# Kernel tuning notes

Measured on AMD Instinct MI355X. Metric: run time of the kernel, lower is better.

## Reference

```python
import jax, jax.numpy as jnp
import numpy as np

PSZ = 3      # patch_size
TOPK = 2     # topk candidates
EPS = 1e-12  # F.normalize eps


def extract_patches(x, psz, stride):
    """Torch unfold-style patch extraction: (B,C,H,W) -> (B, nH*nW, C, psz, psz)."""
    B, C, H, W = x.shape
    nH = (H - psz) // stride + 1
    nW = (W - psz) // stride + 1
    slices = []
    for di in range(psz):          # fixed 3x3 loop, not a data-dim loop
        for dj in range(psz):
            slices.append(x[:, :, di:di + (nH - 1) * stride + 1:stride,
                                  dj:dj + (nW - 1) * stride + 1:stride])
    p = jnp.stack(slices, axis=-1)                      # (B,C,nH,nW,psz*psz)
    p = p.reshape(B, C, nH, nW, psz, psz)
    p = p.transpose(0, 2, 3, 1, 4, 5).reshape(B, nH * nW, C, psz, psz)
    return p


def l2_normalize(x, axis):
    n = jnp.sqrt(jnp.sum(x * x, axis=axis, keepdims=True))
    return x / jnp.maximum(n, EPS)


def setup_inputs() -> dict:
    key = jax.random.key(0)
    k1, k2 = jax.random.split(key)
    pred_style = jax.random.normal(k1, (2, 128, 48, 48), dtype=jnp.float32)
    target_style = jax.random.normal(k2, (2 * TOPK, 128, 48, 48), dtype=jnp.float32)
    return {"pred_style": pred_style, "target_style": target_style}


def reference(pred_style, target_style):
    B = pred_style.shape[0]
    # raw patches (used for the final MSE / gather)
    tp = extract_patches(target_style, PSZ, 1)   # (B*TOPK, nT, C, 3, 3)
    pp = extract_patches(pred_style, PSZ, 1)     # (B, nQ, C, 3, 3)
    nT = tp.shape[1]

    # matching is done on channel-normalized features (F.normalize dim=1 / dim=2)
    p1n = extract_patches(l2_normalize(pred_style, axis=1), PSZ, 1)  # (B,nQ,C,3,3)
    tpn = l2_normalize(tp, axis=2).reshape(B, TOPK, nT, *tp.shape[2:])

    # cosine cross-correlation == conv with candidate patches as filters
    scores = jnp.einsum('bqcij,bkncij->bknq', p1n, tpn)  # (B,TOPK,nT,nQ)->(B,TOPK,nQ) reduce below

    sv = jnp.max(scores, axis=2)      # (B, TOPK, nQ) best value per candidate set
    si = jnp.argmax(scores, axis=2)   # (B, TOPK, nQ) best spatial idx per k
    k_idx = jnp.argmax(sv, axis=1)    # (B, nQ) best k per query position
    spatial = jnp.take_along_axis(si, k_idx[:, None, :], axis=1)[:, 0]  # (B, nQ)

    tpr = tp.reshape(B, TOPK, nT, *tp.shape[2:])
    bi = jnp.arange(B)[:, None]
    gathered = tpr[bi, k_idx, spatial]  # (B, nQ, C, 3, 3)

    return jnp.mean((pp - gathered) ** 2)
```

## Files before the change

kernel.cpp:

```cpp
#include <hip/hip_runtime.h>
#include <hip/hip_bf16.h>

typedef unsigned short u16;
typedef __attribute__((ext_vector_type(8))) short short8;
typedef __attribute__((ext_vector_type(4))) float f32x4;
typedef __attribute__((ext_vector_type(4))) unsigned int u32x4;

#define CC    128
#define WW    48
#define HW2   2304
#define NHW   46
#define NQ    2116
#define NPIX  2304
#define DSTRIDE ((size_t)NPIX * NPIX + 64)
#define BATCH 2

__device__ __forceinline__ u16 f2bf(float f) {
  union { float f; unsigned u; } x; x.f = f;
  unsigned r = (x.u + 0x7fffu + ((x.u >> 16) & 1u)) >> 16;
  return (u16)r;
}
__device__ __forceinline__ float b2f(u16 v) {
  union { unsigned u; float f; } x; x.u = ((unsigned)v) << 16;
  return x.f;
}

__global__ __launch_bounds__(256) void k_norm(const float* __restrict__ pred,
                                              const float* __restrict__ targ,
                                              u16* __restrict__ PnT, u16* __restrict__ TnT) {
  const int img = blockIdx.y;
  const int p0  = blockIdx.x * 64;
  const int tid = threadIdx.x;
  const float* src = img < 2 ? pred + (size_t)img * CC * HW2
                             : targ + (size_t)(img - 2) * CC * HW2;
  u16* out = img < 2 ? PnT + (size_t)img * NPIX * CC
                     : TnT + (size_t)(img - 2) * NPIX * CC;

  __shared__ float sT[64][129];
  __shared__ float sInv[64];

  #pragma unroll
  for (int it = 0; it < 32; ++it) {
    int idx = it * 256 + tid;
    int c = idx >> 6, p = idx & 63;
    sT[p][c] = src[(size_t)c * HW2 + p0 + p];
  }
  __syncthreads();
  if (tid < 64) {
    float s = 0.f;
    for (int c = 0; c < CC; ++c) { float v = sT[tid][c]; s += v * v; }
    sInv[tid] = 1.0f / fmaxf(sqrtf(s), 1e-12f);
  }
  __syncthreads();
  #pragma unroll
  for (int it = 0; it < 4; ++it) {
    int cid = it * 256 + tid;
    int p = cid >> 4, g = cid & 15;
    int r = p0 + p;
    int sc = (g & ~7) | ((g & 7) ^ (r & 7));
    float inv = sInv[p];
    unsigned pack[4];
    #pragma unroll
    for (int e = 0; e < 8; ++e) {
      float v = sT[p][sc * 8 + e] * inv;
      if ((e & 1) == 0) pack[e >> 1] = (unsigned)f2bf(v);
      else              pack[e >> 1] |= ((unsigned)f2bf(v)) << 16;
    }
    u32x4 o; o.x = pack[0]; o.y = pack[1]; o.z = pack[2]; o.w = pack[3];
    *reinterpret_cast<u32x4*>(out + (size_t)r * CC + g * 8) = o;
  }
}

__global__ __launch_bounds__(512) void k_pixdot(const u16* __restrict__ PnT, const u16* __restrict__ TnT,
                                                u16* __restrict__ D) {
  __shared__ u16 sA[128 * 128];
  __shared__ u16 sB[256 * 128];
  const int nt = blockIdx.x, mt = blockIdx.y, s = blockIdx.z;
  const int tid = threadIdx.x, lane = tid & 63, wid = tid >> 6;
  const int wm = wid >> 2, wn = wid & 3;
  const int r15 = lane & 15, g16 = lane >> 4;

  const u16* Ab = PnT + (size_t)(s >> 1) * NPIX * CC + (size_t)mt * 128 * CC;
  const u16* Bb = TnT + (size_t)s * NPIX * CC + (size_t)nt * 256 * CC;
  u16* Dset = D + (size_t)s * DSTRIDE;

  #pragma unroll
  for (int i = 0; i < 4; ++i) {
    int sl = i * 512 + tid;
    __builtin_amdgcn_global_load_lds(
      (const __attribute__((address_space(1))) unsigned*)(Ab + (size_t)(sl >> 4) * CC + (sl & 15) * 8),
      (__attribute__((address_space(3))) unsigned*)&sA[sl * 8], 16, 0, 0);
  }
  #pragma unroll
  for (int i = 0; i < 8; ++i) {
    int sl = i * 512 + tid;
    __builtin_amdgcn_global_load_lds(
      (const __attribute__((address_space(1))) unsigned*)(Bb + (size_t)(sl >> 4) * CC + (sl & 15) * 8),
      (__attribute__((address_space(3))) unsigned*)&sB[sl * 8], 16, 0, 0);
  }

  f32x4 acc[4][4];
  const f32x4 z4 = {0.f, 0.f, 0.f, 0.f};
  #pragma unroll
  for (int i = 0; i < 4; ++i)
    #pragma unroll
    for (int j = 0; j < 4; ++j) acc[i][j] = z4;

  asm volatile("s_waitcnt vmcnt(0)" ::: "memory");
  __builtin_amdgcn_s_barrier();

  const int arow0 = wm * 64 + r15;
  const int brow0 = wn * 64 + r15;
  #pragma unroll
  for (int ks = 0; ks < 4; ++ks) {
    const int c = ks * 4 + g16;
    short8 af[4], bfv[4];
    #pragma unroll
    for (int mi = 0; mi < 4; ++mi) {
      int row = arow0 + mi * 16;
      af[mi] = *reinterpret_cast<const short8*>(
        &sA[row * 128 + (c >> 3) * 64 + (((c & 7) ^ (row & 7)) * 8)]);
    }
    #pragma unroll
    for (int ni = 0; ni < 4; ++ni) {
      int row = brow0 + ni * 16;
      bfv[ni] = *reinterpret_cast<const short8*>(
        &sB[row * 128 + (c >> 3) * 64 + (((c & 7) ^ (row & 7)) * 8)]);
    }
    __builtin_amdgcn_s_setprio(1);
    #pragma unroll
    for (int mi = 0; mi < 4; ++mi)
      #pragma unroll
      for (int ni = 0; ni < 4; ++ni)
        acc[mi][ni] = __builtin_amdgcn_mfma_f32_16x16x32_bf16(af[mi], bfv[ni], acc[mi][ni], 0, 0, 0);
    __builtin_amdgcn_s_setprio(0);
  }

  const int m0 = mt * 128 + wm * 64, n0 = nt * 256 + wn * 64;
  #pragma unroll
  for (int mi = 0; mi < 4; ++mi)
    #pragma unroll
    for (int ni = 0; ni < 4; ++ni)
      #pragma unroll
      for (int rg = 0; rg < 4; ++rg) {
        int row = m0 + mi * 16 + g16 * 4 + rg;
        int col = n0 + ni * 16 + r15;
        Dset[(size_t)row * NPIX + col] = f2bf(acc[mi][ni][rg]);
      }
}

#define HTASKS (2302 * 288)
#define HNB    ((4 * HTASKS) / 256)
__global__ __launch_bounds__(256) void k_hsum(const u16* __restrict__ D, u16* __restrict__ H) {
  const int bid = blockIdx.x;
  const int xcd = bid & 7, pos = bid >> 3;
  const int qch = HNB >> 3, rch = HNB & 7;
  const int sb = (xcd < rch ? xcd * (qch + 1) : rch * (qch + 1) + (xcd - rch) * qch) + pos;
  const int task = sb * 256 + threadIdx.x;
  const int s = task / HTASKS;
  int rem = task - s * HTASKS;
  const int r = rem / 288, c8 = rem - r * 288;

  const u16* Ds = D + (size_t)s * DSTRIDE + (size_t)r * NPIX + c8 * 8;
  u16* Hs = H + (size_t)s * DSTRIDE + (size_t)r * NPIX + c8 * 8;

  short8 a0 = *reinterpret_cast<const short8*>(Ds);
  short8 b0 = *reinterpret_cast<const short8*>(Ds + NPIX);
  short8 b1 = *reinterpret_cast<const short8*>(Ds + NPIX + 8);
  short8 c0 = *reinterpret_cast<const short8*>(Ds + 2 * NPIX);
  short8 c1 = *reinterpret_cast<const short8*>(Ds + 2 * NPIX + 8);
  short8 s1 = __builtin_shufflevector(b0, b1, 1, 2, 3, 4, 5, 6, 7, 8);
  short8 s2 = __builtin_shufflevector(c0, c1, 2, 3, 4, 5, 6, 7, 8, 9);
  unsigned pack[4];
  #pragma unroll
  for (int e = 0; e < 8; ++e) {
    float f = b2f((u16)a0[e]) + b2f((u16)s1[e]) + b2f((u16)s2[e]);
    if ((e & 1) == 0) pack[e >> 1] = (unsigned)f2bf(f);
    else              pack[e >> 1] |= ((unsigned)f2bf(f)) << 16;
  }
  u32x4 o; o.x = pack[0]; o.y = pack[1]; o.z = pack[2]; o.w = pack[3];
  *reinterpret_cast<u32x4*>(Hs) = o;
}

__global__ __launch_bounds__(512) void k_stencil(const u16* __restrict__ H,
                                                 const float* __restrict__ pred,
                                                 const float* __restrict__ targ,
                                                 float* __restrict__ msep) {
  const int bid = blockIdx.x;
  const int b = bid >= NQ ? 1 : 0;
  const int orig = bid - b * NQ;
  const int xcd = orig & 7, pos = orig >> 3;
  const int q = (xcd < 4 ? xcd * 265 : 1060 + (xcd - 4) * 264) + pos;

  const int tid = threadIdx.x, lane = tid & 63, wid = tid >> 6;
  const int qy = q / NHW, qx = q - qy * NHW;
  const int qp = qy * WW + qx;

  float best = -3.0e38f; int bidx = 0x7fffffff;
  #pragma unroll
  for (int it = 0; it < 2; ++it) {
    int t = it * 512 + tid;
    if (t < 552) {
      int kc = t / 276; int rem = t - kc * 276;
      int ny = rem / 6, cx = rem - ny * 6;
      const u16* Hs = H + (size_t)(b * 2 + kc) * DSTRIDE;
      int colb = ny * 48 + cx * 8;
      short8 t0 = *reinterpret_cast<const short8*>(Hs + (size_t)qp * NPIX + colb);
      short8 t1 = *reinterpret_cast<const short8*>(Hs + (size_t)(qp + 48) * NPIX + colb + 48);
      short8 t2 = *reinterpret_cast<const short8*>(Hs + (size_t)(qp + 96) * NPIX + colb + 96);
      int nbase = kc * NQ + ny * NHW + cx * 8;
      #pragma unroll
      for (int e = 0; e < 8; ++e) {
        float sc = b2f((u16)t0[e]) + b2f((u16)t1[e]) + b2f((u16)t2[e]);
        int n = nbase + e;
        bool take = (cx * 8 + e < NHW) &&
                    ((sc > best) || (sc == best && n < bidx));
        best = take ? sc : best;
        bidx = take ? n : bidx;
      }
    }
  }
  #pragma unroll
  for (int off = 1; off < 64; off <<= 1) {
    float ov = __shfl_xor(best, off, 64);
    int   oi = __shfl_xor(bidx, off, 64);
    bool take = (ov > best) || (ov == best && oi < bidx);
    best = take ? ov : best;
    bidx = take ? oi : bidx;
  }

  __shared__ float sv[8]; __shared__ int si[8];
  __shared__ float red[512];
  if (lane == 0) { sv[wid] = best; si[wid] = bidx; }
  __syncthreads();
  float fb = sv[0]; int fi = si[0];
  #pragma unroll
  for (int wv = 1; wv < 8; ++wv) {
    bool take = (sv[wv] > fb) || (sv[wv] == fb && si[wv] < fi);
    fb = take ? sv[wv] : fb;
    fi = take ? si[wv] : fi;
  }

  int nkc = fi >= NQ ? 1 : 0;
  int ns = fi - nkc * NQ;
  int ny = ns / NHW, nx = ns - ny * NHW;
  const float* P = pred + (size_t)b * CC * HW2;
  const float* T = targ + (size_t)(b * 2 + nkc) * CC * HW2;
  float ssum = 0.f;
  for (int i = tid; i < CC * 9; i += 512) {
    int c = i / 9, sp = i - 9 * c;
    int di = sp / 3, dj = sp - 3 * di;
    float d = P[(size_t)c * HW2 + (qy + di) * WW + qx + dj]
            - T[(size_t)c * HW2 + (ny + di) * WW + nx + dj];
    ssum += d * d;
  }
  red[tid] = ssum; __syncthreads();
  for (int st = 256; st > 0; st >>= 1) { if (tid < st) red[tid] += red[tid + st]; __syncthreads(); }
  if (tid == 0) msep[b * NQ + q] = red[0];
}

__global__ void k_final(const float* __restrict__ msep, float* __restrict__ out) {
  int t = threadIdx.x;
  float s = 0.f;
  for (int i = t; i < BATCH * NQ; i += 256) s += msep[i];
  __shared__ float red[256];
  red[t] = s; __syncthreads();
  for (int st = 128; st > 0; st >>= 1) { if (t < st) red[t] += red[t + st]; __syncthreads(); }
  if (t == 0) out[0] = red[0] * (1.0f / 4875264.0f);
}

extern "C" void kernel_launch(void* const* d_in, const int* in_sizes, int n_in,
                              void* d_out, int out_size, void* d_ws, size_t ws_size,
                              hipStream_t stream) {
  const float* pred = (const float*)d_in[0];
  const float* targ = (const float*)d_in[1];
  char* ws = (char*)d_ws;

  size_t offP = 0;
  size_t offT = offP + (size_t)2 * NPIX * CC * 2;
  size_t offD = offT + (size_t)4 * NPIX * CC * 2;
  size_t offH = offD + (size_t)4 * DSTRIDE * 2;
  size_t offM = offH + (size_t)4 * DSTRIDE * 2;

  u16*   PnT  = (u16*)(ws + offP);
  u16*   TnT  = (u16*)(ws + offT);
  u16*   Dbuf = (u16*)(ws + offD);
  u16*   Hbuf = (u16*)(ws + offH);
  float* msep = (float*)(ws + offM);

  k_norm<<<dim3(36, 6), 256, 0, stream>>>(pred, targ, PnT, TnT);
  k_pixdot<<<dim3(9, 18, 4), 512, 0, stream>>>(PnT, TnT, Dbuf);
  k_hsum<<<dim3(HNB), 256, 0, stream>>>(Dbuf, Hbuf);
  k_stencil<<<dim3(BATCH * NQ), 512, 0, stream>>>(Hbuf, pred, targ, msep);
  k_final<<<1, 256, 0, stream>>>(msep, (float*)d_out);
}
```

Measured before the change: 79.99 us.

## Fuse horizontal 3-tap sum into pixel-dot GEMM epilogue via overlapping tiles

```diff
diff --git a/kernel.cpp b/kernel.cpp
--- a/kernel.cpp
+++ b/kernel.cpp
@@ -14,6 +14,8 @@
 #define NPIX  2304
 #define DSTRIDE ((size_t)NPIX * NPIX + 64)
 #define BATCH 2
+#define MT    126
+#define NTC   254
 
 __device__ __forceinline__ u16 f2bf(float f) {
   union { float f; unsigned u; } x; x.f = f;
@@ -71,31 +73,35 @@
   }
 }
 
-__global__ __launch_bounds__(512) void k_pixdot(const u16* __restrict__ PnT, const u16* __restrict__ TnT,
-                                                u16* __restrict__ D) {
-  __shared__ u16 sA[128 * 128];
-  __shared__ u16 sB[256 * 128];
+__global__ __launch_bounds__(512) void k_pixdotH(const u16* __restrict__ PnT, const u16* __restrict__ TnT,
+                                                 u16* __restrict__ H) {
+  __shared__ u16 buf[49152];
+  u16* sA = buf;
+  u16* sB = buf + 16384;
   const int nt = blockIdx.x, mt = blockIdx.y, s = blockIdx.z;
   const int tid = threadIdx.x, lane = tid & 63, wid = tid >> 6;
   const int wm = wid >> 2, wn = wid & 3;
   const int r15 = lane & 15, g16 = lane >> 4;
-
-  const u16* Ab = PnT + (size_t)(s >> 1) * NPIX * CC + (size_t)mt * 128 * CC;
-  const u16* Bb = TnT + (size_t)s * NPIX * CC + (size_t)nt * 256 * CC;
-  u16* Dset = D + (size_t)s * DSTRIDE;
+  const int m0 = mt * MT, n0 = nt * NTC;
+
+  const u16* Ab = PnT + (size_t)(s >> 1) * NPIX * CC;
+  const u16* Bb = TnT + (size_t)s * NPIX * CC;
+  u16* Hs = H + (size_t)s * DSTRIDE;
 
   #pragma unroll
   for (int i = 0; i < 4; ++i) {
     int sl = i * 512 + tid;
+    int row = m0 + (sl >> 4); row = row < 2303 ? row : 2303;
     __builtin_amdgcn_global_load_lds(
-      (const __attribute__((address_space(1))) unsigned*)(Ab + (size_t)(sl >> 4) * CC + (sl & 15) * 8),
+      (const __attribute__((address_space(1))) unsigned*)(Ab + (size_t)row * CC + (sl & 15) * 8),
       (__attribute__((address_space(3))) unsigned*)&sA[sl * 8], 16, 0, 0);
   }
   #pragma unroll
   for (int i = 0; i < 8; ++i) {
     int sl = i * 512 + tid;
+    int row = n0 + (sl >> 4); row = row < 2303 ? row : 2303;
     __builtin_amdgcn_global_load_lds(
-      (const __attribute__((address_space(1))) unsigned*)(Bb + (size_t)(sl >> 4) * CC + (sl & 15) * 8),
+      (const __attribute__((address_space(1))) unsigned*)(Bb + (size_t)row * CC + (sl & 15) * 8),
       (__attribute__((address_space(3))) unsigned*)&sB[sl * 8], 16, 0, 0);
   }
 
@@ -118,14 +124,16 @@
     #pragma unroll
     for (int mi = 0; mi < 4; ++mi) {
       int row = arow0 + mi * 16;
+      int gr = m0 + row;
       af[mi] = *reinterpret_cast<const short8*>(
-        &sA[row * 128 + (c >> 3) * 64 + (((c & 7) ^ (row & 7)) * 8)]);
+        &sA[row * 128 + (c >> 3) * 64 + (((c & 7) ^ (gr & 7)) * 8)]);
     }
     #pragma unroll
     for (int ni = 0; ni < 4; ++ni) {
       int row = brow0 + ni * 16;
+      int gr = n0 + row;
       bfv[ni] = *reinterpret_cast<const short8*>(
-        &sB[row * 128 + (c >> 3) * 64 + (((c & 7) ^ (row & 7)) * 8)]);
+        &sB[row * 128 + (c >> 3) * 64 + (((c & 7) ^ (gr & 7)) * 8)]);
     }
     __builtin_amdgcn_s_setprio(1);
     #pragma unroll
@@ -136,50 +144,51 @@
     __builtin_amdgcn_s_setprio(0);
   }
 
-  const int m0 = mt * 128 + wm * 64, n0 = nt * 256 + wn * 64;
+  __syncthreads();
+  u16* Dt = buf;
   #pragma unroll
   for (int mi = 0; mi < 4; ++mi)
     #pragma unroll
-    for (int ni = 0; ni < 4; ++ni)
+    for (int ni = 0; ni < 4; ++ni) {
+      int col = wn * 64 + ni * 16 + r15;
       #pragma unroll
       for (int rg = 0; rg < 4; ++rg) {
-        int row = m0 + mi * 16 + g16 * 4 + rg;
-        int col = n0 + ni * 16 + r15;
-        Dset[(size_t)row * NPIX + col] = f2bf(acc[mi][ni][rg]);
+        int row = wm * 64 + mi * 16 + g16 * 4 + rg;
+        Dt[row * 256 + col] = f2bf(acc[mi][ni][rg]);
       }
-}
-
-#define HTASKS (2302 * 288)
-#define HNB    ((4 * HTASKS) / 256)
-__global__ __launch_bounds__(256) void k_hsum(const u16* __restrict__ D, u16* __restrict__ H) {
-  const int bid = blockIdx.x;
-  const int xcd = bid & 7, pos = bid >> 3;
-  const int qch = HNB >> 3, rch = HNB & 7;
-  const int sb = (xcd < rch ? xcd * (qch + 1) : rch * (qch + 1) + (xcd - rch) * qch) + pos;
-  const int task = sb * 256 + threadIdx.x;
-  const int s = task / HTASKS;
-  int rem = task - s * HTASKS;
-  const int r = rem / 288, c8 = rem - r * 288;
-
-  const u16* Ds = D + (size_t)s * DSTRIDE + (size_t)r * NPIX + c8 * 8;
-  u16* Hs = H + (size_t)s * DSTRIDE + (size_t)r * NPIX + c8 * 8;
-
-  short8 a0 = *reinterpret_cast<const short8*>(Ds);
-  short8 b0 = *reinterpret_cast<const short8*>(Ds + NPIX);
-  short8 b1 = *reinterpret_cast<const short8*>(Ds + NPIX + 8);
-  short8 c0 = *reinterpret_cast<const short8*>(Ds + 2 * NPIX);
-  short8 c1 = *reinterpret_cast<const short8*>(Ds + 2 * NPIX + 8);
-  short8 s1 = __builtin_shufflevector(b0, b1, 1, 2, 3, 4, 5, 6, 7, 8);
-  short8 s2 = __builtin_shufflevector(c0, c1, 2, 3, 4, 5, 6, 7, 8, 9);
-  unsigned pack[4];
-  #pragma unroll
-  for (int e = 0; e < 8; ++e) {
-    float f = b2f((u16)a0[e]) + b2f((u16)s1[e]) + b2f((u16)s2[e]);
-    if ((e & 1) == 0) pack[e >> 1] = (unsigned)f2bf(f);
-    else              pack[e >> 1] |= ((unsigned)f2bf(f)) << 16;
-  }
-  u32x4 o; o.x = pack[0]; o.y = pack[1]; o.z = pack[2]; o.w = pack[3];
-  *reinterpret_cast<u32x4*>(Hs) = o;
+    }
+  __syncthreads();
+
+  for (int t = tid; t < 4032; t += 512) {
+    int rr = t >> 5, c8 = t & 31;
+    int grow = m0 + rr;
+    if (grow >= 2302) continue;
+    int lcol = c8 * 8;
+    int lim = 254 - lcol;
+    int glim = 2302 - (n0 + lcol);
+    lim = lim < glim ? lim : glim;
+    if (lim <= 0) continue;
+    int base = rr * 256 + lcol;
+    short8 a0 = *reinterpret_cast<const short8*>(&Dt[base]);
+    short8 b0 = *reinterpret_cast<const short8*>(&Dt[base + 256]);
+    short8 b1 = *reinterpret_cast<const short8*>(&Dt[base + 264]);
+    short8 c0 = *reinterpret_cast<const short8*>(&Dt[base + 512]);
+    short8 c1 = *reinterpret_cast<const short8*>(&Dt[base + 520]);
+    short8 s1v = __builtin_shufflevector(b0, b1, 1, 2, 3, 4, 5, 6, 7, 8);
+    short8 s2v = __builtin_shufflevector(c0, c1, 2, 3, 4, 5, 6, 7, 8, 9);
+    unsigned pack[4];
+    #pragma unroll
+    for (int e = 0; e < 8; ++e) {
+      float f = b2f((u16)a0[e]) + b2f((u16)s1v[e]) + b2f((u16)s2v[e]);
+      if ((e & 1) == 0) pack[e >> 1] = (unsigned)f2bf(f);
+      else              pack[e >> 1] |= ((unsigned)f2bf(f)) << 16;
+    }
+    u16* dst = Hs + (size_t)grow * NPIX + n0 + lcol;
+    int nd = lim >= 8 ? 4 : ((lim + 1) >> 1);
+    #pragma unroll
+    for (int d = 0; d < 4; ++d)
+      if (d < nd) *reinterpret_cast<unsigned*>(dst + 2 * d) = pack[d];
+  }
 }
 
 __global__ __launch_bounds__(512) void k_stencil(const u16* __restrict__ H,
@@ -278,19 +287,16 @@
 
   size_t offP = 0;
   size_t offT = offP + (size_t)2 * NPIX * CC * 2;
-  size_t offD = offT + (size_t)4 * NPIX * CC * 2;
-  size_t offH = offD + (size_t)4 * DSTRIDE * 2;
+  size_t offH = offT + (size_t)4 * NPIX * CC * 2;
   size_t offM = offH + (size_t)4 * DSTRIDE * 2;
 
   u16*   PnT  = (u16*)(ws + offP);
   u16*   TnT  = (u16*)(ws + offT);
-  u16*   Dbuf = (u16*)(ws + offD);
   u16*   Hbuf = (u16*)(ws + offH);
   float* msep = (float*)(ws + offM);
 
   k_norm<<<dim3(36, 6), 256, 0, stream>>>(pred, targ, PnT, TnT);
-  k_pixdot<<<dim3(9, 18, 4), 512, 0, stream>>>(PnT, TnT, Dbuf);
-  k_hsum<<<dim3(HNB), 256, 0, stream>>>(Dbuf, Hbuf);
+  k_pixdotH<<<dim3(10, 19, 4), 512, 0, stream>>>(PnT, TnT, Hbuf);
   k_stencil<<<dim3(BATCH * NQ), 512, 0, stream>>>(Hbuf, pred, targ, msep);
   k_final<<<1, 256, 0, stream>>>(msep, (float*)d_out);
 }
```

Result: faster. 77.50 us (-3.1%).
